# Kernel tuning notes

Hardware: AMD Instinct MI355X
Metric: run time of the kernel (lower is better)

Reference implementation:

```python
import jax, jax.numpy as jnp
import numpy as np

B, S, D = 2, 2048, 1024
H, HD = 16, 64

def setup_inputs() -> dict:
    key = jax.random.key(0)
    k1, k2, k3 = jax.random.split(key, 3)
    x = jax.random.normal(k1, (B, S, D), dtype=jnp.float32)
    w_qkv = jax.random.normal(k2, (3 * D, D), dtype=jnp.float32) * (D ** -0.5)
    w_out = jax.random.normal(k3, (D, D), dtype=jnp.float32) * (D ** -0.5)
    return {"x": x, "w_qkv": w_qkv, "w_out": w_out}

def reference(x, w_qkv, w_out):
    scale = HD ** -0.5
    # qkv projection: torch Linear applies x @ W.T
    qkv = jnp.einsum('bsd,ed->bse', x, w_qkv)            # [B,S,3D]
    qkv = qkv.reshape(B, S, 3, H, HD)
    q, k, v = qkv[:, :, 0], qkv[:, :, 1], qkv[:, :, 2]   # [B,S,H,HD]
    # scores: explicit matmul-softmax-matmul (unfused, as in source)
    scores = jnp.einsum('bqhd,bkhd->bhqk', q, k) * scale  # [B,H,S,S]
    attn = jax.nn.softmax(scores, axis=-1)
    out = jnp.einsum('bhqk,bkhd->bqhd', attn, v)          # [B,S,H,HD]
    out = out.reshape(B, S, D)
    return jnp.einsum('bsd,ed->bse', out, w_out)
```

## Files before the change

### kernel.cpp

```cpp
#include <hip/hip_runtime.h>
#include <hip/hip_bf16.h>
#include <math.h>

#define B_ 2
#define S_ 2048
#define D_ 1024
#define H_ 16
#define HD_ 64

typedef short bf16x8 __attribute__((ext_vector_type(8)));
typedef short bf16x4 __attribute__((ext_vector_type(4)));
typedef float f32x4 __attribute__((ext_vector_type(4)));

#define MFMA32(a, b, c) __builtin_amdgcn_mfma_f32_16x16x32_bf16(a, b, c, 0, 0, 0)
#define MFMA16(a, b, c) __builtin_amdgcn_mfma_f32_16x16x16bf16_1k(a, b, c, 0, 0, 0)

static __device__ __forceinline__ unsigned short f2bf(float f) {
    union { float f; unsigned u; } v = {f};
    return (unsigned short)((v.u + 0x7fffu + ((v.u >> 16) & 1u)) >> 16);
}

static __device__ __forceinline__ unsigned pk2bf(float a, float b) {
    __hip_bfloat162 h = __float22bfloat162_rn(make_float2(a, b));
    unsigned r;
    __builtin_memcpy(&r, &h, 4);
    return r;
}

static __device__ __forceinline__ void gl2lds16(const void* g, void* l) {
    __builtin_amdgcn_global_load_lds((const __attribute__((address_space(1))) unsigned int*)g,
                                     (__attribute__((address_space(3))) unsigned int*)l,
                                     16, 0, 0);
}

static __device__ __forceinline__ bf16x8 scaleQ(bf16x8 v, float s) {
    union { bf16x8 v; unsigned u[4]; } a, r;
    a.v = v;
    #pragma unroll
    for (int i = 0; i < 4; ++i) {
        float lo = __uint_as_float(a.u[i] << 16);
        float hi = __uint_as_float(a.u[i] & 0xffff0000u);
        r.u[i] = pk2bf(lo * s, hi * s);
    }
    return r.v;
}

__global__ __launch_bounds__(256) void cvt_all(const float* __restrict__ x,
                                               const float* __restrict__ wq,
                                               const float* __restrict__ wo,
                                               unsigned short* __restrict__ xb,
                                               unsigned short* __restrict__ wqb,
                                               unsigned short* __restrict__ wob) {
    const int N0 = 1048576, N1 = 786432, N2 = 262144;
    int stride = gridDim.x * blockDim.x;
    for (int i = blockIdx.x * blockDim.x + threadIdx.x; i < N0 + N1 + N2; i += stride) {
        const float4* src; ushort4* dst; int j;
        if (i < N0)            { src = (const float4*)x;  dst = (ushort4*)xb;  j = i; }
        else if (i < N0 + N1)  { src = (const float4*)wq; dst = (ushort4*)wqb; j = i - N0; }
        else                   { src = (const float4*)wo; dst = (ushort4*)wob; j = i - N0 - N1; }
        float4 v = src[j];
        ushort4 o;
        o.x = f2bf(v.x); o.y = f2bf(v.y); o.z = f2bf(v.z); o.w = f2bf(v.w);
        dst[j] = o;
    }
}

template <int BN>
__global__ __launch_bounds__(256) void gemm_nt_b(const unsigned short* __restrict__ A,
                                                 const unsigned short* __restrict__ Bm,
                                                 void* __restrict__ Cout,
                                                 int M, int N, int K, int c_bf16) {
    constexpr int BM = 128, BK = 32;
    constexpr int MI = (BN == 128) ? 4 : 2;
    constexpr int NI = 4;
    constexpr int SEGS = (BM + BN) / 16;
    __shared__ unsigned short As[BM * BK];
    __shared__ unsigned short Bs[BN * BK];

    const int tid = threadIdx.x;
    const int wave = tid >> 6, lane = tid & 63;
    const int m16 = lane & 15, quad = lane >> 4;
    const int wrow = (BN == 128) ? (wave >> 1) * 64 : wave * 32;
    const int wcol = (BN == 128) ? (wave & 1) * 64 : 0;
    const int row0 = blockIdx.y * BM, col0 = blockIdx.x * BN;

    const int lrow = lane >> 2;
    const int lk = (lane & 3) * 8;

    f32x4 acc[MI][NI] = {};

    for (int k0 = 0; k0 < K; k0 += BK) {
        __syncthreads();
        for (int s = wave; s < SEGS; s += 4) {
            if (s < BM / 16) {
                gl2lds16(&A[(size_t)(row0 + s * 16 + lrow) * K + k0 + lk],
                         &As[s * 16 * BK]);
            } else {
                int t = s - BM / 16;
                gl2lds16(&Bm[(size_t)(col0 + t * 16 + lrow) * K + k0 + lk],
                         &Bs[t * 16 * BK]);
            }
        }
        __asm__ volatile("s_waitcnt vmcnt(0)" ::: "memory");
        __syncthreads();

        bf16x8 af[MI], bfr[NI];
        #pragma unroll
        for (int mi = 0; mi < MI; ++mi)
            af[mi] = *(const bf16x8*)&As[(wrow + mi * 16 + m16) * BK + quad * 8];
        #pragma unroll
        for (int ni = 0; ni < NI; ++ni)
            bfr[ni] = *(const bf16x8*)&Bs[(wcol + ni * 16 + m16) * BK + quad * 8];
        #pragma unroll
        for (int mi = 0; mi < MI; ++mi)
            #pragma unroll
            for (int ni = 0; ni < NI; ++ni)
                acc[mi][ni] = MFMA32(af[mi], bfr[ni], acc[mi][ni]);
    }

    #pragma unroll
    for (int mi = 0; mi < MI; ++mi) {
        #pragma unroll
        for (int r = 0; r < 4; ++r) {
            size_t grow = row0 + wrow + mi * 16 + quad * 4 + r;
            #pragma unroll
            for (int ni = 0; ni < NI; ++ni) {
                size_t gcol = col0 + wcol + ni * 16 + m16;
                if (c_bf16)
                    ((unsigned short*)Cout)[grow * N + gcol] = f2bf(acc[mi][ni][r]);
                else
                    ((float*)Cout)[grow * N + gcol] = acc[mi][ni][r];
            }
        }
    }
}

__global__ __launch_bounds__(256) void transpose_v(const unsigned short* __restrict__ qkv,
                                                   unsigned short* __restrict__ vt) {
    __shared__ unsigned short T[64 * 72];
    const int bid = blockIdx.x;
    const int bh = bid & 31, st = bid >> 5;
    const int b = bh >> 4, h = bh & 15;
    const int tid = threadIdx.x;

    #pragma unroll
    for (int i = 0; i < 2; ++i) {
        int idx = tid + i * 256;
        int r = idx >> 3, c8 = (idx & 7) * 8;
        *(uint4*)&T[r * 72 + c8] =
            *(const uint4*)(qkv + (size_t)(b * S_ + st * 64 + r) * (3 * D_) + 2 * D_ + h * HD_ + c8);
    }
    __syncthreads();
    #pragma unroll
    for (int i = 0; i < 2; ++i) {
        int idx = tid + i * 256;
        int d = idx >> 3, s8 = (idx & 7) * 8;
        unsigned short a[8];
        #pragma unroll
        for (int j = 0; j < 8; ++j) a[j] = T[(s8 + j) * 72 + d];
        *(uint4*)(vt + ((size_t)bh * 64 + d) * S_ + st * 64 + s8) = *(uint4*)a;
    }
}

__global__ __launch_bounds__(256) void attn_mfma(const unsigned short* __restrict__ qkv,
                                                 const unsigned short* __restrict__ vt,
                                                 unsigned short* __restrict__ out) {
    __shared__ unsigned short Ks[2][128 * 64];
    __shared__ unsigned short Vs[2][128 * 64];

    const int id = blockIdx.x;
    const int bh = ((id >> 3) & 3) * 8 + (id & 7);
    const int b = bh >> 4, h = bh & 15;
    const int q0 = (id >> 5) * 128;

    const int tid = threadIdx.x;
    const int wave = tid >> 6, lane = tid & 63;
    const int m16 = lane & 15, quad = lane >> 4;

    const float QS = 0.125f * 1.44269504089f;

    bf16x8 qf0[2], qf1[2];
    #pragma unroll
    for (int g = 0; g < 2; ++g) {
        const unsigned short* qrow =
            qkv + ((size_t)b * S_ + q0 + wave * 32 + g * 16 + m16) * (3 * D_) + h * HD_;
        qf0[g] = scaleQ(*(const bf16x8*)(qrow + quad * 8), QS);
        qf1[g] = scaleQ(*(const bf16x8*)(qrow + 32 + quad * 8), QS);
    }

    f32x4 o[2][4] = {};
    f32x4 ol[2] = {};
    const bf16x4 onesf = {(short)0x3F80, (short)0x3F80, (short)0x3F80, (short)0x3F80};

    const unsigned short* kbase = qkv + (size_t)b * S_ * 3 * D_ + D_ + h * HD_;
    const unsigned short* vtbase = vt + (size_t)bh * 64 * S_;

    const int lr8 = lane >> 3;
    const int lsrc = (lane & 7) ^ lr8;

    int vaddr[4][4];
    #pragma unroll
    for (int dt = 0; dt < 4; ++dt) {
        int d = dt * 16 + m16;
        #pragma unroll
        for (int nt = 0; nt < 4; ++nt) {
            int kc = nt * 2 + (quad >> 1);
            vaddr[dt][nt] = d * 64 + ((kc ^ (m16 & 7)) * 8) + (quad & 1) * 4;
        }
    }

    auto issueDMA = [&](int t, int buf) {
        const unsigned short* kt = kbase + (size_t)t * 128 * (3 * D_);
        const unsigned short* vtt = vtbase + t * 128;
        #pragma unroll
        for (int i = 0; i < 4; ++i) {
            int gi = wave * 4 + i;
            int r = gi * 8 + lr8;
            gl2lds16(kt + (size_t)r * (3 * D_) + lsrc * 8, &Ks[buf][gi * 512]);
            int panel = gi >> 3, vd = (gi & 7) * 8 + lr8;
            gl2lds16(vtt + (size_t)vd * S_ + panel * 64 + lsrc * 8, &Vs[buf][gi * 512]);
        }
    };

    issueDMA(0, 0);
    __asm__ volatile("s_waitcnt vmcnt(0)" ::: "memory");
    __syncthreads();
    issueDMA(1, 1);

    for (int t = 0; t < S_ / 128; ++t) {
        const int buf = t & 1;

        #pragma unroll
        for (int h2 = 0; h2 < 2; ++h2) {
            const unsigned short* Kp = &Ks[buf][h2 * 4096];
            const unsigned short* Vp = &Vs[buf][h2 * 4096];

            bf16x4 pf[2][4];
            #pragma unroll
            for (int nt = 0; nt < 4; ++nt) {
                int a0 = (nt * 16 + m16) * 64 + ((quad ^ (m16 & 7)) * 8);
                bf16x8 kf0 = *(const bf16x8*)&Kp[a0];
                bf16x8 kf1 = *(const bf16x8*)&Kp[a0 ^ 32];
                #pragma unroll
                for (int g = 0; g < 2; ++g) {
                    f32x4 z = {0.f, 0.f, 0.f, 0.f};
                    z = MFMA32(kf0, qf0[g], z);
                    z = MFMA32(kf1, qf1[g], z);
                    float p0 = __builtin_amdgcn_exp2f(z[0]);
                    float p1 = __builtin_amdgcn_exp2f(z[1]);
                    float p2 = __builtin_amdgcn_exp2f(z[2]);
                    float p3 = __builtin_amdgcn_exp2f(z[3]);
                    union { unsigned u[2]; bf16x4 v; } pk;
                    pk.u[0] = pk2bf(p0, p1);
                    pk.u[1] = pk2bf(p2, p3);
                    pf[g][nt] = pk.v;
                    ol[g] = MFMA16(pf[g][nt], onesf, ol[g]);
                }
            }

            #pragma unroll
            for (int nt = 0; nt < 4; ++nt)
                #pragma unroll
                for (int dt = 0; dt < 4; ++dt) {
                    bf16x4 vf = *(const bf16x4*)&Vp[vaddr[dt][nt]];
                    o[0][dt] = MFMA16(pf[0][nt], vf, o[0][dt]);
                    o[1][dt] = MFMA16(pf[1][nt], vf, o[1][dt]);
                }
        }

        __asm__ volatile("s_waitcnt vmcnt(0)" ::: "memory");
        __syncthreads();
        if (t + 2 < S_ / 128) issueDMA(t + 2, buf);
    }

    #pragma unroll
    for (int g = 0; g < 2; ++g)
        #pragma unroll
        for (int r = 0; r < 4; ++r) {
            float inv = 1.f / ol[g][r];
            size_t row = (size_t)b * S_ + q0 + wave * 32 + g * 16 + quad * 4 + r;
            unsigned short* op = out + row * D_ + h * HD_;
            #pragma unroll
            for (int dt = 0; dt < 4; ++dt)
                op[dt * 16 + m16] = f2bf(o[g][dt][r] * inv);
        }
}

extern "C" void kernel_launch(void* const* d_in, const int* in_sizes, int n_in,
                              void* d_out, int out_size, void* d_ws, size_t ws_size,
                              hipStream_t stream) {
    const float* x     = (const float*)d_in[0];
    const float* w_qkv = (const float*)d_in[1];
    const float* w_out = (const float*)d_in[2];
    float* out = (float*)d_out;

    const size_t n_x = (size_t)B_ * S_ * D_;
    const size_t n_wqkv = (size_t)3 * D_ * D_;
    const size_t n_wout = (size_t)D_ * D_;

    unsigned short* xb    = (unsigned short*)d_ws;
    unsigned short* wqkvb = xb + n_x;
    unsigned short* woutb = wqkvb + n_wqkv;
    unsigned short* qkvb  = woutb + n_wout;
    unsigned short* attnb = qkvb + (size_t)B_ * S_ * 3 * D_;
    unsigned short* vtb   = attnb + n_x;

    dim3 blk(256);

    cvt_all<<<2048, blk, 0, stream>>>(x, w_qkv, w_out, xb, wqkvb, woutb);

    gemm_nt_b<128><<<dim3(3 * D_ / 128, B_ * S_ / 128), blk, 0, stream>>>(
        xb, wqkvb, qkvb, B_ * S_, 3 * D_, D_, 1);

    transpose_v<<<1024, blk, 0, stream>>>(qkvb, vtb);

    attn_mfma<<<512, blk, 0, stream>>>(qkvb, vtb, attnb);

    gemm_nt_b<64><<<dim3(D_ / 64, B_ * S_ / 128), blk, 0, stream>>>(
        attnb, woutb, out, B_ * S_, D_, D_, 0);
}
```

Before: 205.3 us.

## Double-buffer GEMM shared tiles to overlap global-to-LDS loads with MFMA

The NT GEMM now keeps two LDS buffers per operand and issues the load for the tile two steps ahead while computing on the current one, so DMA latency can hide behind MFMA work. This doubles the GEMM's LDS footprint, which may lower occupancy. Separately, the fp32-to-bf16 conversion kernel now packs pairs with a hardware packed convert and writes uint2 instead of four scalar rounding conversions.

```diff
diff --git a/kernel.cpp b/kernel.cpp
--- a/kernel.cpp
+++ b/kernel.cpp
@@ -54,13 +54,14 @@
     const int N0 = 1048576, N1 = 786432, N2 = 262144;
     int stride = gridDim.x * blockDim.x;
     for (int i = blockIdx.x * blockDim.x + threadIdx.x; i < N0 + N1 + N2; i += stride) {
-        const float4* src; ushort4* dst; int j;
-        if (i < N0)            { src = (const float4*)x;  dst = (ushort4*)xb;  j = i; }
-        else if (i < N0 + N1)  { src = (const float4*)wq; dst = (ushort4*)wqb; j = i - N0; }
-        else                   { src = (const float4*)wo; dst = (ushort4*)wob; j = i - N0 - N1; }
+        const float4* src; uint2* dst; int j;
+        if (i < N0)            { src = (const float4*)x;  dst = (uint2*)xb;  j = i; }
+        else if (i < N0 + N1)  { src = (const float4*)wq; dst = (uint2*)wqb; j = i - N0; }
+        else                   { src = (const float4*)wo; dst = (uint2*)wob; j = i - N0 - N1; }
         float4 v = src[j];
-        ushort4 o;
-        o.x = f2bf(v.x); o.y = f2bf(v.y); o.z = f2bf(v.z); o.w = f2bf(v.w);
+        uint2 o;
+        o.x = pk2bf(v.x, v.y);
+        o.y = pk2bf(v.z, v.w);
         dst[j] = o;
     }
 }
@@ -74,8 +75,8 @@
     constexpr int MI = (BN == 128) ? 4 : 2;
     constexpr int NI = 4;
     constexpr int SEGS = (BM + BN) / 16;
-    __shared__ unsigned short As[BM * BK];
-    __shared__ unsigned short Bs[BN * BK];
+    __shared__ unsigned short As[2][BM * BK];
+    __shared__ unsigned short Bs[2][BN * BK];
 
     const int tid = threadIdx.x;
     const int wave = tid >> 6, lane = tid & 63;
@@ -89,33 +90,44 @@
 
     f32x4 acc[MI][NI] = {};
 
-    for (int k0 = 0; k0 < K; k0 += BK) {
-        __syncthreads();
+    auto issueDMA = [&](int k0, int buf) {
         for (int s = wave; s < SEGS; s += 4) {
             if (s < BM / 16) {
                 gl2lds16(&A[(size_t)(row0 + s * 16 + lrow) * K + k0 + lk],
-                         &As[s * 16 * BK]);
+                         &As[buf][s * 16 * BK]);
             } else {
                 int t = s - BM / 16;
                 gl2lds16(&Bm[(size_t)(col0 + t * 16 + lrow) * K + k0 + lk],
-                         &Bs[t * 16 * BK]);
+                         &Bs[buf][t * 16 * BK]);
             }
         }
+    };
+
+    issueDMA(0, 0);
+    __asm__ volatile("s_waitcnt vmcnt(0)" ::: "memory");
+    __syncthreads();
+    issueDMA(BK, 1);
+
+    const int NIT = K / BK;
+    for (int it = 0; it < NIT; ++it) {
+        const int buf = it & 1;
+
+        bf16x8 af[MI], bfr[NI];
+        #pragma unroll
+        for (int mi = 0; mi < MI; ++mi)
+            af[mi] = *(const bf16x8*)&As[buf][(wrow + mi * 16 + m16) * BK + quad * 8];
+        #pragma unroll
+        for (int ni = 0; ni < NI; ++ni)
+            bfr[ni] = *(const bf16x8*)&Bs[buf][(wcol + ni * 16 + m16) * BK + quad * 8];
+        #pragma unroll
+        for (int mi = 0; mi < MI; ++mi)
+            #pragma unroll
+            for (int ni = 0; ni < NI; ++ni)
+                acc[mi][ni] = MFMA32(af[mi], bfr[ni], acc[mi][ni]);
+
         __asm__ volatile("s_waitcnt vmcnt(0)" ::: "memory");
         __syncthreads();
-
-        bf16x8 af[MI], bfr[NI];
-        #pragma unroll
-        for (int mi = 0; mi < MI; ++mi)
-            af[mi] = *(const bf16x8*)&As[(wrow + mi * 16 + m16) * BK + quad * 8];
-        #pragma unroll
-        for (int ni = 0; ni < NI; ++ni)
-            bfr[ni] = *(const bf16x8*)&Bs[(wcol + ni * 16 + m16) * BK + quad * 8];
-        #pragma unroll
-        for (int mi = 0; mi < MI; ++mi)
-            #pragma unroll
-            for (int ni = 0; ni < NI; ++ni)
-                acc[mi][ni] = MFMA32(af[mi], bfr[ni], acc[mi][ni]);
+        if (it + 2 < NIT) issueDMA((it + 2) * BK, buf);
     }
 
     #pragma unroll
```

After: 211.1 us. +2.8%, slower.
